# Optimization experiments

Measured on AMD Instinct MI355X. Metric: run time of the kernel, lower is better.

## Reference

```python
import jax, jax.numpy as jnp
import numpy as np

MARGIN = 0.3  # init_kwargs
EPS = 1e-12   # torch F.normalize eps


def _pairwise_dist(f):
    # Euclidean cdist via the stable quadratic expansion; f is [B, D].
    sq = jnp.sum(f * f, axis=1)                      # [B]
    d2 = sq[:, None] + sq[None, :] - 2.0 * (f @ f.T)  # [B, B]
    d2 = jnp.maximum(d2, 0.0)
    # safe sqrt: zero distance (diagonal / duplicates) -> 0 with zero grad
    pos = d2 > 0.0
    return jnp.sqrt(jnp.where(pos, d2, 1.0)) * pos


def reference(features, labels):
    B = features.shape[0]
    norm = jnp.linalg.norm(features, axis=1, keepdims=True)
    f = features / jnp.maximum(norm, EPS)            # F.normalize(dim=1)

    dist = _pairwise_dist(f)                         # [B, B]
    mask = labels[:, None] == labels[None, :]        # positives (incl. self)

    pos_count = jnp.sum(mask, axis=1)                # [B], >= 1 (self)
    has_pos = pos_count > 1                          # needs another positive
    has_neg = pos_count < B                          # at least one negative
    valid = has_pos & has_neg

    # mean over positive distances (includes the self-distance 0, as in torch code)
    mean_pos = jnp.sum(dist * mask, axis=1) / pos_count.astype(dist.dtype)  # [B]

    # semi-hard negatives: negatives with dist > mean positive dist
    sh_mask = (~mask) & (dist > mean_pos[:, None])   # [B, B]
    has_sh = jnp.any(sh_mask, axis=1)
    min_sh = jnp.min(jnp.where(sh_mask, dist, jnp.inf), axis=1)
    min_sh = jnp.where(has_sh, min_sh, 0.0)          # guard inf for invalid rows

    contrib = valid & has_sh
    per_anchor = jax.nn.relu(mean_pos - min_sh + MARGIN)
    loss_sum = jnp.sum(jnp.where(contrib, per_anchor, 0.0))
    count = jnp.sum(contrib)
    return jnp.where(count > 0, loss_sum / count.astype(dist.dtype), 0.0)


def setup_inputs() -> dict:
    key = jax.random.key(0)
    k1, k2 = jax.random.split(key)
    features = jax.random.normal(k1, (8192, 512), dtype=jnp.float32)
    labels = jax.random.randint(k2, (8192,), 0, 128, dtype=jnp.int64)
    return {"features": features, "labels": labels}
```

## Files before the change

kernel.cpp:

```cpp
#include <hip/hip_runtime.h>
#include <math.h>

#define EPS_N 1e-12f
#define MARGIN 0.3f
#define INF_BITS 0x7f800000u
#define NCLS 128
#define D 512
#define PADR 256

typedef __attribute__((ext_vector_type(8))) short short8;
typedef __attribute__((ext_vector_type(4))) float float4v;

__device__ __forceinline__ unsigned short f2bf(float f) {
    unsigned u = __float_as_uint(f);
    u += 0x7fff + ((u >> 16) & 1);
    return (unsigned short)(u >> 16);
}
__device__ __forceinline__ void gl16(const void* g, void* l) {
    __builtin_amdgcn_global_load_lds((const __attribute__((address_space(1))) void*)g,
                                     (__attribute__((address_space(3))) void*)l, 16, 0, 0);
}

__global__ __launch_bounds__(1024) void k_bucket(const int* __restrict__ lab, int Bn,
        int* __restrict__ pos, int* __restrict__ labp,
        int* __restrict__ cstart_g, int* __restrict__ ccnt_g,
        float* __restrict__ meanpos, float* __restrict__ pcinv,
        int* __restrict__ poscnt, unsigned* __restrict__ minbits) {
    __shared__ int cnt[NCLS], cs[NCLS + 1], off[NCLS], sa[NCLS], sb[NCLS];
    int tid = threadIdx.x;
    if (tid < NCLS) cnt[tid] = 0;
    __syncthreads();
    for (int i = tid; i < Bn; i += 1024) atomicAdd(&cnt[lab[i] & (NCLS - 1)], 1);
    __syncthreads();
    if (tid < NCLS) sa[tid] = cnt[tid];
    __syncthreads();
    int* src = sa; int* dst = sb;
    for (int ofs = 1; ofs < NCLS; ofs <<= 1) {
        if (tid < NCLS) dst[tid] = src[tid] + ((tid >= ofs) ? src[tid - ofs] : 0);
        __syncthreads();
        int* t = src; src = dst; dst = t;
    }
    if (tid < NCLS) {
        int ex = src[tid] - cnt[tid];
        cs[tid] = ex;
        off[tid] = ex;
        cstart_g[tid] = ex;
        ccnt_g[tid] = cnt[tid];
    }
    if (tid == 0) cs[NCLS] = Bn;
    __syncthreads();
    for (int p = tid; p < Bn; p += 1024) {
        int lo = 0, hi = NCLS - 1;
        #pragma unroll
        for (int s = 0; s < 7; ++s) {
            int mid = (lo + hi + 1) >> 1;
            if (cs[mid] <= p) lo = mid; else hi = mid - 1;
        }
        int l = lo, m = cnt[l];
        labp[p] = l;
        poscnt[p] = m;
        pcinv[p] = 1.0f / (float)m;
        meanpos[p] = 0.f;
        minbits[p] = INF_BITS;
    }
    for (int i = tid; i < Bn; i += 1024) {
        int l = lab[i] & (NCLS - 1);
        pos[i] = atomicAdd(&off[l], 1);
    }
}

__global__ __launch_bounds__(256) void k_normalize(const float* __restrict__ x,
        const int* __restrict__ pos, unsigned short* __restrict__ fh,
        float* __restrict__ sqp) {
    int w = threadIdx.x >> 6, L = threadIdx.x & 63;
    int row = blockIdx.x * 4 + w;
    const float* xr = x + (size_t)row * D + L * 8;
    float4 a = *(const float4*)xr;
    float4 b = *(const float4*)(xr + 4);
    float ss = a.x * a.x;
    ss = fmaf(a.y, a.y, ss); ss = fmaf(a.z, a.z, ss); ss = fmaf(a.w, a.w, ss);
    ss = fmaf(b.x, b.x, ss); ss = fmaf(b.y, b.y, ss);
    ss = fmaf(b.z, b.z, ss); ss = fmaf(b.w, b.w, ss);
    #pragma unroll
    for (int off = 32; off; off >>= 1) ss += __shfl_xor(ss, off, 64);
    float inv = 1.0f / fmaxf(sqrtf(ss), EPS_N);
    int prow = pos[row];
    if (L == 0) sqp[prow] = ss * inv * inv;
    ushort4 h0, h1;
    h0.x = f2bf(a.x * inv); h0.y = f2bf(a.y * inv);
    h0.z = f2bf(a.z * inv); h0.w = f2bf(a.w * inv);
    h1.x = f2bf(b.x * inv); h1.y = f2bf(b.y * inv);
    h1.z = f2bf(b.z * inv); h1.w = f2bf(b.w * inv);
    unsigned short* dst = fh + (size_t)prow * D + L * 8;
    *(ushort4*)dst = h0;
    *(ushort4*)(dst + 4) = h1;
}

__global__ __launch_bounds__(256) void k_posclass(
    const unsigned short* __restrict__ fh, const float* __restrict__ sqp,
    const int* __restrict__ cstart_g, const int* __restrict__ ccnt_g,
    float* __restrict__ meanpos)
{
    const int c = blockIdx.x;
    const int s = cstart_g[c], n = ccnt_g[c];
    if (n <= 1) return;

    __shared__ unsigned short SA[128 * 128];
    __shared__ unsigned short SB[128 * 128];
    __shared__ float sqr_sh[128], sqs[128], rs[128];

    const int tid = threadIdx.x, w = tid >> 6, L = tid & 63;
    const int lm = L & 15, ls = L >> 4;

    for (int rb = 0; rb < n; rb += 128) {
        const int nr = min(128, n - rb);
        __syncthreads();
        if (tid < 128) {
            rs[tid] = 0.f;
            sqr_sh[tid] = (tid < nr) ? sqp[s + rb + tid] : 0.f;
        }
        for (int cb = 0; cb < n; cb += 128) {
            const int m = min(128, n - cb);
            const bool same = (rb == cb);
            __syncthreads();
            if (tid < 128) sqs[tid] = (tid < m) ? sqp[s + cb + tid] : 0.f;

            float4v acc[8][2];
            #pragma unroll
            for (int rt = 0; rt < 8; ++rt)
                #pragma unroll
                for (int ct = 0; ct < 2; ++ct) acc[rt][ct] = (float4v){0.f, 0.f, 0.f, 0.f};

            for (int k0 = 0; k0 < D; k0 += 128) {
                __syncthreads();
                #pragma unroll
                for (int q = 0; q < 8; ++q) {
                    int slot = tid + 256 * q;
                    int r = slot >> 4;
                    int u = (slot & 15) ^ (r & 15);
                    if (r < nr)
                        gl16(fh + (size_t)(s + rb + r) * D + k0 + u * 8,
                             &SA[(w * 64 + 256 * q) * 8]);
                }
                if (!same) {
                    #pragma unroll
                    for (int q = 0; q < 8; ++q) {
                        int slot = tid + 256 * q;
                        int r = slot >> 4;
                        int u = (slot & 15) ^ (r & 15);
                        if (r < m)
                            gl16(fh + (size_t)(s + cb + r) * D + k0 + u * 8,
                                 &SB[(w * 64 + 256 * q) * 8]);
                    }
                }
                __syncthreads();
                const unsigned short* Bb = same ? SA : SB;
                #pragma unroll
                for (int h = 0; h < 4; ++h) {
                    short8 bf[2];
                    #pragma unroll
                    for (int ct = 0; ct < 2; ++ct) {
                        int cr = w * 32 + ct * 16 + lm;
                        bf[ct] = *(const short8*)&Bb[cr * 128 + (((h * 4 + ls) ^ (cr & 15))) * 8];
                    }
                    #pragma unroll
                    for (int rt = 0; rt < 8; ++rt) {
                        int ar = rt * 16 + lm;
                        short8 af = *(const short8*)&SA[ar * 128 + (((h * 4 + ls) ^ (ar & 15))) * 8];
                        #pragma unroll
                        for (int ct = 0; ct < 2; ++ct)
                            acc[rt][ct] = __builtin_amdgcn_mfma_f32_16x16x32_bf16(af, bf[ct], acc[rt][ct], 0, 0, 0);
                    }
                }
            }
            #pragma unroll
            for (int rt = 0; rt < 8; ++rt) {
                #pragma unroll
                for (int v = 0; v < 4; ++v) {
                    int ri = rt * 16 + ls * 4 + v;
                    float sr = sqr_sh[ri];
                    float sum = 0.f;
                    #pragma unroll
                    for (int ct = 0; ct < 2; ++ct) {
                        int ci = w * 32 + ct * 16 + lm;
                        float d2 = sr + sqs[ci] - 2.0f * acc[rt][ct][v];
                        bool ok = (ri < nr) && (ci < m) && (rb + ri != cb + ci) && (d2 > 0.f);
                        sum += ok ? sqrtf(d2) : 0.f;
                    }
                    #pragma unroll
                    for (int off = 8; off; off >>= 1) sum += __shfl_xor(sum, off, 64);
                    if (lm == 0 && sum != 0.f) atomicAdd(&rs[ri], sum);
                }
            }
        }
        __syncthreads();
        if (tid < nr) meanpos[s + rb + tid] = rs[tid];
    }
}

#define BKG 64

__global__ __launch_bounds__(256, 4) void k_minsh_mfma(
    const unsigned short* __restrict__ fh, const float* __restrict__ sqp,
    const int* __restrict__ labp, const float* __restrict__ meanpos,
    const float* __restrict__ pcinv, unsigned* __restrict__ minbits)
{
    int t = (blockIdx.x & 7) * 260 + (blockIdx.x >> 3);
    int rq = (int)((sqrtf(8.0f * (float)t + 1.0f) - 1.0f) * 0.5f);
    while ((rq + 1) * (rq + 2) / 2 <= t) ++rq;
    while (rq * (rq + 1) / 2 > t) --rq;
    int cq = t - rq * (rq + 1) / 2;
    const int i0 = cq * 128, j0 = rq * 128;
    const bool diag = (i0 == j0);

    __shared__ unsigned short LA[2][128 * BKG];
    __shared__ float s_mp2r[128], s_mp2c[128], s_sqr[128], s_sqc[128];
    __shared__ int s_labr[128], s_labc[128];

    const int tid = threadIdx.x;
    const int w = tid >> 6, L = tid & 63;

    if (tid < 128) {
        float mp = meanpos[i0 + tid] * pcinv[i0 + tid];
        s_mp2r[tid] = mp * mp;
        s_sqr[tid]  = sqp[i0 + tid];
        s_labr[tid] = labp[i0 + tid];
    } else {
        int q = tid - 128;
        float mp = meanpos[j0 + q] * pcinv[j0 + q];
        s_mp2c[q] = mp * mp;
        s_sqc[q]  = sqp[j0 + q];
        s_labc[q] = labp[j0 + q];
    }

    const unsigned short* msrc = fh + (size_t)((w < 2) ? i0 : j0) * D;
    unsigned short* mylds = &LA[(w < 2) ? 0 : 1][(w & 1) * 64 * BKG];
    const int srow = L >> 3;
    const int sseg = L & 7;

    float4v acc[4][4];
    #pragma unroll
    for (int a = 0; a < 4; ++a)
        #pragma unroll
        for (int bq = 0; bq < 4; ++bq) acc[a][bq] = (float4v){0.f, 0.f, 0.f, 0.f};

    const int rw = (w >> 1) * 64, cw = (w & 1) * 64;
    const int lm = L & 15, ls = L >> 4;

    for (int k0 = 0; k0 < D; k0 += BKG) {
        __syncthreads();
        #pragma unroll
        for (int it = 0; it < 8; ++it) {
            int rmat = (w & 1) * 64 + it * 8 + srow;
            int seg = sseg ^ (rmat & 7);
            gl16(msrc + (size_t)rmat * D + k0 + seg * 8, mylds + it * 512);
        }
        __syncthreads();
        #pragma unroll
        for (int h = 0; h < 2; ++h) {
            short8 ah[4], bh[4];
            #pragma unroll
            for (int mi = 0; mi < 4; ++mi) {
                int r = rw + mi * 16 + lm;
                int slot = r * 8 + ((h * 4 + ls) ^ (r & 7));
                ah[mi] = *(const short8*)&LA[0][slot * 8];
            }
            #pragma unroll
            for (int ni = 0; ni < 4; ++ni) {
                int cc = cw + ni * 16 + lm;
                int slot = cc * 8 + ((h * 4 + ls) ^ (cc & 7));
                bh[ni] = *(const short8*)&LA[1][slot * 8];
            }
            #pragma unroll
            for (int ni = 0; ni < 4; ++ni)
                #pragma unroll
                for (int mi = 0; mi < 4; ++mi)
                    acc[mi][ni] = __builtin_amdgcn_mfma_f32_16x16x32_bf16(ah[mi], bh[ni], acc[mi][ni], 0, 0, 0);
        }
    }

    const float INFF = __uint_as_float(INF_BITS);
    float sc[4], mp2c[4];
    int lc[4];
    #pragma unroll
    for (int ni = 0; ni < 4; ++ni) {
        int cl = cw + ni * 16 + lm;
        sc[ni]   = s_sqc[cl];
        mp2c[ni] = s_mp2c[cl];
        lc[ni]   = s_labc[cl];
    }
    float vminc[4];
    #pragma unroll
    for (int ni = 0; ni < 4; ++ni) vminc[ni] = INFF;

    #pragma unroll
    for (int mi = 0; mi < 4; ++mi) {
        #pragma unroll
        for (int v = 0; v < 4; ++v) {
            int rl = rw + mi * 16 + ls * 4 + v;
            float mp2r = s_mp2r[rl];
            float sr   = s_sqr[rl];
            int   li   = s_labr[rl];
            float vminr = INFF;
            #pragma unroll
            for (int ni = 0; ni < 4; ++ni) {
                float d2 = fmaf(-2.0f, acc[mi][ni][v], sr + sc[ni]);
                bool neq = (li != lc[ni]);
                vminr     = fminf(vminr,     (neq && d2 > mp2r)     ? d2 : INFF);
                vminc[ni] = fminf(vminc[ni], (neq && d2 > mp2c[ni]) ? d2 : INFF);
            }
            #pragma unroll
            for (int off = 8; off; off >>= 1)
                vminr = fminf(vminr, __shfl_xor(vminr, off, 64));
            if (lm == 0 && __float_as_uint(vminr) != INF_BITS)
                atomicMin(&minbits[i0 + rl], __float_as_uint(vminr));
        }
    }
    if (!diag) {
        #pragma unroll
        for (int ni = 0; ni < 4; ++ni) {
            float vc = vminc[ni];
            vc = fminf(vc, __shfl_xor(vc, 16, 64));
            vc = fminf(vc, __shfl_xor(vc, 32, 64));
            if (ls == 0 && __float_as_uint(vc) != INF_BITS)
                atomicMin(&minbits[j0 + cw + ni * 16 + lm], __float_as_uint(vc));
        }
    }
}

__global__ __launch_bounds__(1024) void k_finish(const float* __restrict__ meanpos,
        const float* __restrict__ pcinv, const int* __restrict__ poscnt,
        const unsigned* __restrict__ minbits, float* __restrict__ out, int Bn) {
    float lsum = 0.f; int lcnt = 0;
    for (int i = threadIdx.x; i < Bn; i += 1024) {
        int pc = poscnt[i];
        bool valid = (pc > 1) && (pc < Bn);
        unsigned mb = minbits[i];
        if (valid && mb != INF_BITS) {
            float v = fmaf(meanpos[i], pcinv[i], MARGIN - sqrtf(__uint_as_float(mb)));
            lsum += (v > 0.f) ? v : 0.f;
            lcnt += 1;
        }
    }
    __shared__ float ssum[16]; __shared__ int scnt[16];
    int lane = threadIdx.x & 63, wid = threadIdx.x >> 6;
    #pragma unroll
    for (int off = 32; off; off >>= 1) {
        lsum += __shfl_down(lsum, off, 64);
        lcnt += __shfl_down(lcnt, off, 64);
    }
    if (lane == 0) { ssum[wid] = lsum; scnt[wid] = lcnt; }
    __syncthreads();
    if (threadIdx.x == 0) {
        float s = 0.f; int c = 0;
        #pragma unroll
        for (int q = 0; q < 16; ++q) { s += ssum[q]; c += scnt[q]; }
        out[0] = (c > 0) ? s / (float)c : 0.f;
    }
}

extern "C" void kernel_launch(void* const* d_in, const int* in_sizes, int n_in,
                              void* d_out, int out_size, void* d_ws, size_t ws_size,
                              hipStream_t stream) {
    const float* x = (const float*)d_in[0];
    const int* lab = (const int*)d_in[1];
    int Bn = in_sizes[1];

    size_t nd = (size_t)(Bn + PADR) * D;
    unsigned short* fh = (unsigned short*)d_ws;
    float* sqp        = (float*)(fh + nd);
    float* meanpos    = sqp + Bn;
    float* pcinv      = meanpos + Bn;
    int* poscnt       = (int*)(pcinv + Bn);
    unsigned* minbits = (unsigned*)(poscnt + Bn);
    int* pos          = (int*)(minbits + Bn);
    int* labp         = pos + Bn;
    int* cstart_g     = labp + Bn;
    int* ccnt_g       = cstart_g + NCLS;

    k_bucket<<<1, 1024, 0, stream>>>(lab, Bn, pos, labp, cstart_g, ccnt_g,
                                     meanpos, pcinv, poscnt, minbits);
    k_normalize<<<Bn / 4, 256, 0, stream>>>(x, pos, fh, sqp);
    k_posclass<<<NCLS, 256, 0, stream>>>(fh, sqp, cstart_g, ccnt_g, meanpos);
    int nb = Bn / 128;
    int T = nb * (nb + 1) / 2;
    k_minsh_mfma<<<T, 256, 0, stream>>>(fh, sqp, labp, meanpos, pcinv, minbits);
    k_finish<<<1, 1024, 0, stream>>>(meanpos, pcinv, poscnt, minbits,
                                     (float*)d_out, Bn);
}
```

Before: 162.7 us.

## Quantize normalized features to int8 and use i8 MFMA for Gram products

```diff
diff --git a/kernel.cpp b/kernel.cpp
--- a/kernel.cpp
+++ b/kernel.cpp
@@ -9,13 +9,10 @@
 #define PADR 256
 
 typedef __attribute__((ext_vector_type(8))) short short8;
+typedef __attribute__((ext_vector_type(8))) char  char8;
+typedef __attribute__((ext_vector_type(4))) int   int4x;
 typedef __attribute__((ext_vector_type(4))) float float4v;
 
-__device__ __forceinline__ unsigned short f2bf(float f) {
-    unsigned u = __float_as_uint(f);
-    u += 0x7fff + ((u >> 16) & 1);
-    return (unsigned short)(u >> 16);
-}
 __device__ __forceinline__ void gl16(const void* g, void* l) {
     __builtin_amdgcn_global_load_lds((const __attribute__((address_space(1))) void*)g,
                                      (__attribute__((address_space(3))) void*)l, 16, 0, 0);
@@ -70,8 +67,8 @@
 }
 
 __global__ __launch_bounds__(256) void k_normalize(const float* __restrict__ x,
-        const int* __restrict__ pos, unsigned short* __restrict__ fh,
-        float* __restrict__ sqp) {
+        const int* __restrict__ pos, char* __restrict__ fh8,
+        float* __restrict__ qs, float* __restrict__ sqp) {
     int w = threadIdx.x >> 6, L = threadIdx.x & 63;
     int row = blockIdx.x * 4 + w;
     const float* xr = x + (size_t)row * D + L * 8;
@@ -84,30 +81,42 @@
     #pragma unroll
     for (int off = 32; off; off >>= 1) ss += __shfl_xor(ss, off, 64);
     float inv = 1.0f / fmaxf(sqrtf(ss), EPS_N);
+    float e0 = a.x * inv, e1 = a.y * inv, e2 = a.z * inv, e3 = a.w * inv;
+    float e4 = b.x * inv, e5 = b.y * inv, e6 = b.z * inv, e7 = b.w * inv;
+    float mv = fmaxf(fmaxf(fmaxf(fabsf(e0), fabsf(e1)), fmaxf(fabsf(e2), fabsf(e3))),
+                     fmaxf(fmaxf(fabsf(e4), fabsf(e5)), fmaxf(fabsf(e6), fabsf(e7))));
+    #pragma unroll
+    for (int off = 32; off; off >>= 1) mv = fmaxf(mv, __shfl_xor(mv, off, 64));
+    float r127 = 127.0f / mv;
     int prow = pos[row];
-    if (L == 0) sqp[prow] = ss * inv * inv;
-    ushort4 h0, h1;
-    h0.x = f2bf(a.x * inv); h0.y = f2bf(a.y * inv);
-    h0.z = f2bf(a.z * inv); h0.w = f2bf(a.w * inv);
-    h1.x = f2bf(b.x * inv); h1.y = f2bf(b.y * inv);
-    h1.z = f2bf(b.z * inv); h1.w = f2bf(b.w * inv);
-    unsigned short* dst = fh + (size_t)prow * D + L * 8;
-    *(ushort4*)dst = h0;
-    *(ushort4*)(dst + 4) = h1;
+    if (L == 0) {
+        sqp[prow] = ss * inv * inv;
+        qs[prow]  = mv * (1.0f / 127.0f);
+    }
+    char8 pk;
+    pk[0] = (char)__float2int_rn(e0 * r127);
+    pk[1] = (char)__float2int_rn(e1 * r127);
+    pk[2] = (char)__float2int_rn(e2 * r127);
+    pk[3] = (char)__float2int_rn(e3 * r127);
+    pk[4] = (char)__float2int_rn(e4 * r127);
+    pk[5] = (char)__float2int_rn(e5 * r127);
+    pk[6] = (char)__float2int_rn(e6 * r127);
+    pk[7] = (char)__float2int_rn(e7 * r127);
+    *(char8*)(fh8 + (size_t)prow * D + L * 8) = pk;
 }
 
 __global__ __launch_bounds__(256) void k_posclass(
-    const unsigned short* __restrict__ fh, const float* __restrict__ sqp,
-    const int* __restrict__ cstart_g, const int* __restrict__ ccnt_g,
-    float* __restrict__ meanpos)
+    const char* __restrict__ fh8, const float* __restrict__ sqp,
+    const float* __restrict__ qs, const int* __restrict__ cstart_g,
+    const int* __restrict__ ccnt_g, float* __restrict__ meanpos)
 {
     const int c = blockIdx.x;
     const int s = cstart_g[c], n = ccnt_g[c];
     if (n <= 1) return;
 
-    __shared__ unsigned short SA[128 * 128];
-    __shared__ unsigned short SB[128 * 128];
-    __shared__ float sqr_sh[128], sqs[128], rs[128];
+    __shared__ char SA[128 * 128];
+    __shared__ char SB[128 * 128];
+    __shared__ float sqr_sh[128], sqs[128], rs[128], qsr_sh[128], qss[128];
 
     const int tid = threadIdx.x, w = tid >> 6, L = tid & 63;
     const int lm = L & 15, ls = L >> 4;
@@ -118,58 +127,62 @@
         if (tid < 128) {
             rs[tid] = 0.f;
             sqr_sh[tid] = (tid < nr) ? sqp[s + rb + tid] : 0.f;
+            qsr_sh[tid] = (tid < nr) ? qs[s + rb + tid] : 0.f;
         }
         for (int cb = 0; cb < n; cb += 128) {
             const int m = min(128, n - cb);
             const bool same = (rb == cb);
             __syncthreads();
-            if (tid < 128) sqs[tid] = (tid < m) ? sqp[s + cb + tid] : 0.f;
-
-            float4v acc[8][2];
+            if (tid < 128) {
+                sqs[tid] = (tid < m) ? sqp[s + cb + tid] : 0.f;
+                qss[tid] = (tid < m) ? qs[s + cb + tid] : 0.f;
+            }
+
+            int4x acc[8][2];
             #pragma unroll
             for (int rt = 0; rt < 8; ++rt)
                 #pragma unroll
-                for (int ct = 0; ct < 2; ++ct) acc[rt][ct] = (float4v){0.f, 0.f, 0.f, 0.f};
+                for (int ct = 0; ct < 2; ++ct) acc[rt][ct] = (int4x){0, 0, 0, 0};
 
             for (int k0 = 0; k0 < D; k0 += 128) {
                 __syncthreads();
                 #pragma unroll
-                for (int q = 0; q < 8; ++q) {
+                for (int q = 0; q < 4; ++q) {
                     int slot = tid + 256 * q;
-                    int r = slot >> 4;
-                    int u = (slot & 15) ^ (r & 15);
+                    int r = slot >> 3;
+                    int u = (slot & 7) ^ (r & 7);
                     if (r < nr)
-                        gl16(fh + (size_t)(s + rb + r) * D + k0 + u * 8,
-                             &SA[(w * 64 + 256 * q) * 8]);
+                        gl16(fh8 + (size_t)(s + rb + r) * D + k0 + u * 16,
+                             &SA[(size_t)slot * 16]);
                 }
                 if (!same) {
                     #pragma unroll
-                    for (int q = 0; q < 8; ++q) {
+                    for (int q = 0; q < 4; ++q) {
                         int slot = tid + 256 * q;
-                        int r = slot >> 4;
-                        int u = (slot & 15) ^ (r & 15);
+                        int r = slot >> 3;
+                        int u = (slot & 7) ^ (r & 7);
                         if (r < m)
-                            gl16(fh + (size_t)(s + cb + r) * D + k0 + u * 8,
-                                 &SB[(w * 64 + 256 * q) * 8]);
+                            gl16(fh8 + (size_t)(s + cb + r) * D + k0 + u * 16,
+                                 &SB[(size_t)slot * 16]);
                     }
                 }
                 __syncthreads();
-                const unsigned short* Bb = same ? SA : SB;
+                const char* Bb = same ? SA : SB;
                 #pragma unroll
-                for (int h = 0; h < 4; ++h) {
-                    short8 bf[2];
+                for (int h = 0; h < 2; ++h) {
+                    int4x bf[2];
                     #pragma unroll
                     for (int ct = 0; ct < 2; ++ct) {
                         int cr = w * 32 + ct * 16 + lm;
-                        bf[ct] = *(const short8*)&Bb[cr * 128 + (((h * 4 + ls) ^ (cr & 15))) * 8];
+                        bf[ct] = *(const int4x*)&Bb[cr * 128 + (((h * 4 + ls) ^ (cr & 7))) * 16];
                     }
                     #pragma unroll
                     for (int rt = 0; rt < 8; ++rt) {
                         int ar = rt * 16 + lm;
-                        short8 af = *(const short8*)&SA[ar * 128 + (((h * 4 + ls) ^ (ar & 15))) * 8];
+                        int4x af = *(const int4x*)&SA[ar * 128 + (((h * 4 + ls) ^ (ar & 7))) * 16];
                         #pragma unroll
                         for (int ct = 0; ct < 2; ++ct)
-                            acc[rt][ct] = __builtin_amdgcn_mfma_f32_16x16x32_bf16(af, bf[ct], acc[rt][ct], 0, 0, 0);
+                            acc[rt][ct] = __builtin_amdgcn_mfma_i32_16x16x64_i8(af, bf[ct], acc[rt][ct], 0, 0, 0);
                     }
                 }
             }
@@ -179,11 +192,13 @@
                 for (int v = 0; v < 4; ++v) {
                     int ri = rt * 16 + ls * 4 + v;
                     float sr = sqr_sh[ri];
+                    float qr = qsr_sh[ri];
                     float sum = 0.f;
                     #pragma unroll
                     for (int ct = 0; ct < 2; ++ct) {
                         int ci = w * 32 + ct * 16 + lm;
-                        float d2 = sr + sqs[ci] - 2.0f * acc[rt][ct][v];
+                        float dot = (float)acc[rt][ct][v] * qr * qss[ci];
+                        float d2 = sr + sqs[ci] - 2.0f * dot;
                         bool ok = (ri < nr) && (ci < m) && (rb + ri != cb + ci) && (d2 > 0.f);
                         sum += ok ? sqrtf(d2) : 0.f;
                     }
@@ -198,12 +213,11 @@
     }
 }
 
-#define BKG 64
-
 __global__ __launch_bounds__(256, 4) void k_minsh_mfma(
-    const unsigned short* __restrict__ fh, const float* __restrict__ sqp,
-    const int* __restrict__ labp, const float* __restrict__ meanpos,
-    const float* __restrict__ pcinv, unsigned* __restrict__ minbits)
+    const char* __restrict__ fh8, const float* __restrict__ sqp,
+    const float* __restrict__ qs, const int* __restrict__ labp,
+    const float* __restrict__ meanpos, const float* __restrict__ pcinv,
+    unsigned* __restrict__ minbits)
 {
     int t = (blockIdx.x & 7) * 260 + (blockIdx.x >> 3);
     int rq = (int)((sqrtf(8.0f * (float)t + 1.0f) - 1.0f) * 0.5f);
@@ -213,8 +227,9 @@
     const int i0 = cq * 128, j0 = rq * 128;
     const bool diag = (i0 == j0);
 
-    __shared__ unsigned short LA[2][128 * BKG];
+    __shared__ char LA[2][128 * 128];
     __shared__ float s_mp2r[128], s_mp2c[128], s_sqr[128], s_sqc[128];
+    __shared__ float s_qsr[128], s_qsc[128];
     __shared__ int s_labr[128], s_labc[128];
 
     const int tid = threadIdx.x;
@@ -224,69 +239,72 @@
         float mp = meanpos[i0 + tid] * pcinv[i0 + tid];
         s_mp2r[tid] = mp * mp;
         s_sqr[tid]  = sqp[i0 + tid];
+        s_qsr[tid]  = qs[i0 + tid];
         s_labr[tid] = labp[i0 + tid];
     } else {
         int q = tid - 128;
         float mp = meanpos[j0 + q] * pcinv[j0 + q];
         s_mp2c[q] = mp * mp;
         s_sqc[q]  = sqp[j0 + q];
+        s_qsc[q]  = qs[j0 + q];
         s_labc[q] = labp[j0 + q];
     }
 
-    const unsigned short* msrc = fh + (size_t)((w < 2) ? i0 : j0) * D;
-    unsigned short* mylds = &LA[(w < 2) ? 0 : 1][(w & 1) * 64 * BKG];
+    const char* msrc = fh8 + (size_t)((w < 2) ? i0 : j0) * D;
+    char* mylds = &LA[(w < 2) ? 0 : 1][(w & 1) * 64 * 128];
     const int srow = L >> 3;
     const int sseg = L & 7;
 
-    float4v acc[4][4];
+    int4x acc[4][4];
     #pragma unroll
     for (int a = 0; a < 4; ++a)
         #pragma unroll
-        for (int bq = 0; bq < 4; ++bq) acc[a][bq] = (float4v){0.f, 0.f, 0.f, 0.f};
+        for (int bq = 0; bq < 4; ++bq) acc[a][bq] = (int4x){0, 0, 0, 0};
 
     const int rw = (w >> 1) * 64, cw = (w & 1) * 64;
     const int lm = L & 15, ls = L >> 4;
 
-    for (int k0 = 0; k0 < D; k0 += BKG) {
+    for (int k0 = 0; k0 < D; k0 += 128) {
         __syncthreads();
         #pragma unroll
         for (int it = 0; it < 8; ++it) {
             int rmat = (w & 1) * 64 + it * 8 + srow;
             int seg = sseg ^ (rmat & 7);
-            gl16(msrc + (size_t)rmat * D + k0 + seg * 8, mylds + it * 512);
+            gl16(msrc + (size_t)rmat * D + k0 + seg * 16, mylds + it * 1024);
         }
         __syncthreads();
         #pragma unroll
         for (int h = 0; h < 2; ++h) {
-            short8 ah[4], bh[4];
+            int4x ah[4], bh[4];
             #pragma unroll
             for (int mi = 0; mi < 4; ++mi) {
                 int r = rw + mi * 16 + lm;
                 int slot = r * 8 + ((h * 4 + ls) ^ (r & 7));
-                ah[mi] = *(const short8*)&LA[0][slot * 8];
+                ah[mi] = *(const int4x*)&LA[0][slot * 16];
             }
             #pragma unroll
             for (int ni = 0; ni < 4; ++ni) {
                 int cc = cw + ni * 16 + lm;
                 int slot = cc * 8 + ((h * 4 + ls) ^ (cc & 7));
-                bh[ni] = *(const short8*)&LA[1][slot * 8];
+                bh[ni] = *(const int4x*)&LA[1][slot * 16];
             }
             #pragma unroll
             for (int ni = 0; ni < 4; ++ni)
                 #pragma unroll
                 for (int mi = 0; mi < 4; ++mi)
-                    acc[mi][ni] = __builtin_amdgcn_mfma_f32_16x16x32_bf16(ah[mi], bh[ni], acc[mi][ni], 0, 0, 0);
+                    acc[mi][ni] = __builtin_amdgcn_mfma_i32_16x16x64_i8(ah[mi], bh[ni], acc[mi][ni], 0, 0, 0);
         }
     }
 
     const float INFF = __uint_as_float(INF_BITS);
-    float sc[4], mp2c[4];
+    float sc[4], mp2c[4], qc[4];
     int lc[4];
     #pragma unroll
     for (int ni = 0; ni < 4; ++ni) {
         int cl = cw + ni * 16 + lm;
         sc[ni]   = s_sqc[cl];
         mp2c[ni] = s_mp2c[cl];
+        qc[ni]   = s_qsc[cl];
         lc[ni]   = s_labc[cl];
     }
     float vminc[4];
@@ -300,11 +318,13 @@
             int rl = rw + mi * 16 + ls * 4 + v;
             float mp2r = s_mp2r[rl];
             float sr   = s_sqr[rl];
+            float qr   = s_qsr[rl];
             int   li   = s_labr[rl];
             float vminr = INFF;
             #pragma unroll
             for (int ni = 0; ni < 4; ++ni) {
-                float d2 = fmaf(-2.0f, acc[mi][ni][v], sr + sc[ni]);
+                float dot = (float)acc[mi][ni][v] * qr * qc[ni];
+                float d2 = fmaf(-2.0f, dot, sr + sc[ni]);
                 bool neq = (li != lc[ni]);
                 vminr     = fminf(vminr,     (neq && d2 > mp2r)     ? d2 : INFF);
                 vminc[ni] = fminf(vminc[ni], (neq && d2 > mp2c[ni]) ? d2 : INFF);
@@ -366,10 +386,11 @@
     const int* lab = (const int*)d_in[1];
     int Bn = in_sizes[1];
 
-    size_t nd = (size_t)(Bn + PADR) * D;
-    unsigned short* fh = (unsigned short*)d_ws;
-    float* sqp        = (float*)(fh + nd);
-    float* meanpos    = sqp + Bn;
+    size_t nd8 = (size_t)(Bn + PADR) * D;
+    char* fh8         = (char*)d_ws;
+    float* sqp        = (float*)(fh8 + nd8);
+    float* qsv        = sqp + Bn;
+    float* meanpos    = qsv + Bn;
     float* pcinv      = meanpos + Bn;
     int* poscnt       = (int*)(pcinv + Bn);
     unsigned* minbits = (unsigned*)(poscnt + Bn);
@@ -380,11 +401,11 @@
 
     k_bucket<<<1, 1024, 0, stream>>>(lab, Bn, pos, labp, cstart_g, ccnt_g,
                                      meanpos, pcinv, poscnt, minbits);
-    k_normalize<<<Bn / 4, 256, 0, stream>>>(x, pos, fh, sqp);
-    k_posclass<<<NCLS, 256, 0, stream>>>(fh, sqp, cstart_g, ccnt_g, meanpos);
+    k_normalize<<<Bn / 4, 256, 0, stream>>>(x, pos, fh8, qsv, sqp);
+    k_posclass<<<NCLS, 256, 0, stream>>>(fh8, sqp, qsv, cstart_g, ccnt_g, meanpos);
     int nb = Bn / 128;
     int T = nb * (nb + 1) / 2;
-    k_minsh_mfma<<<T, 256, 0, stream>>>(fh, sqp, labp, meanpos, pcinv, minbits);
+    k_minsh_mfma<<<T, 256, 0, stream>>>(fh8, sqp, qsv, labp, meanpos, pcinv, minbits);
     k_finish<<<1, 1024, 0, stream>>>(meanpos, pcinv, poscnt, minbits,
                                      (float*)d_out, Bn);
 }
```

Result: faster. 145.4 us (-10.6%).
